# Optimization experiments

Measured on AMD Instinct MI355X. Metric: run time of the kernel, lower is better.

The kernel has to match this reference:

```python
import jax, jax.numpy as jnp
import numpy as np


def _gelu(x):
    # torch nn.GELU default is the exact (erf) variant
    return jax.nn.gelu(x, approximate=False)


def setup_inputs() -> dict:
    key = jax.random.key(0)
    ks = jax.random.split(key, 10)
    B, IN, H, D, C, K = 32768, 64, 256, 16, 8, 64
    HS = D // 2  # structure_filter hidden (latent_dim > 2)

    def rn(k, shape, scale):
        return jax.random.normal(k, shape, dtype=jnp.float32) * scale

    x = rn(ks[0], (B, IN), 1.0)
    W1 = rn(ks[1], (IN, H), 1.0 / np.sqrt(IN)); b1 = jnp.zeros((H,), jnp.float32)
    W2 = rn(ks[2], (H, H), 1.0 / np.sqrt(H));   b2 = jnp.zeros((H,), jnp.float32)
    Wv = rn(ks[3], (H, D), 1.0 / np.sqrt(H));   bv = jnp.zeros((D,), jnp.float32)
    chart_centers = rn(ks[4], (C, D), 0.02)
    codebook = rn(ks[5], (C, K, D), 0.02)
    sf_W1 = rn(ks[6], (D, HS), 1.0 / np.sqrt(D));  sf_b1 = jnp.zeros((HS,), jnp.float32)
    sf_W2 = rn(ks[7], (HS, D), 1.0 / np.sqrt(HS)); sf_b2 = jnp.zeros((D,), jnp.float32)
    return {
        "x": x, "W1": W1, "b1": b1, "W2": W2, "b2": b2, "Wv": Wv, "bv": bv,
        "chart_centers": chart_centers, "codebook": codebook,
        "sf_W1": sf_W1, "sf_b1": sf_b1, "sf_W2": sf_W2, "sf_b2": sf_b2,
    }


def reference(x, W1, b1, W2, b2, Wv, bv, chart_centers, codebook, sf_W1, sf_b1, sf_W2, sf_b2):
    sg = jax.lax.stop_gradient
    # feature extractor: Linear -> GELU -> Linear -> GELU
    f = _gelu(x @ W1 + b1)
    f = _gelu(f @ W2 + b2)
    v = f @ Wv + bv                                        # [B, D]
    D = v.shape[-1]
    C = codebook.shape[0]
    # chart routing
    scores = (v @ chart_centers.T) / jnp.sqrt(jnp.float32(D))   # [B, C]
    router_weights = jax.nn.softmax(scores, axis=-1)
    K_chart = jnp.argmax(router_weights, axis=1)                 # [B]
    c_bar = router_weights @ chart_centers                       # [B, D]
    v_local = v - c_bar
    # per-chart codebook distances
    diff = v_local[:, None, None, :] - codebook[None]            # [B, C, K, D]
    dist = jnp.sum(diff * diff, axis=-1)                         # [B, C, K]
    indices = jnp.argmin(dist, axis=-1)                          # [B, C]
    z_q_all = codebook[jnp.arange(C)[None, :], indices]          # [B, C, D]
    # VQ losses (router weights detached)
    w = sg(router_weights)[:, :, None]                           # [B, C, 1]
    v_bc = v_local[:, None, :]                                   # [B, 1, D]
    commitment = jnp.sum(jnp.mean((v_bc - sg(z_q_all)) ** 2 * w, axis=(0, 2)))
    codebook_loss = jnp.sum(jnp.mean((z_q_all - sg(v_bc)) ** 2 * w, axis=(0, 2)))
    vq_loss = codebook_loss + 0.25 * commitment
    z_q_blended = jnp.sum(z_q_all * router_weights[:, :, None], axis=1)   # [B, D]
    K_code = jnp.take_along_axis(indices, K_chart[:, None], axis=1)[:, 0]  # [B]
    # structure filter on per-chart residuals
    delta = v_bc - sg(z_q_all)                                   # [B, C, D]
    z_n_all_charts = _gelu(delta @ sf_W1 + sf_b1) @ sf_W2 + sf_b2  # [B, C, D]
    z_n = jnp.sum(z_n_all_charts * router_weights[:, :, None], axis=1)
    z_tex = (v_local - sg(z_q_blended)) - z_n
    z_q_st = v_local + sg(z_q_blended - v_local)                 # straight-through
    z_geo = c_bar + z_q_st + z_n
    return (K_chart, K_code, z_n, z_tex, router_weights, z_geo, vq_loss,
            indices, z_n_all_charts, c_bar)
```

## Files before the change

### kernel.cpp

```cpp
#include <hip/hip_runtime.h>
#include <hip/hip_bf16.h>

#define O0 0ull
#define O1 32768ull
#define O2 65536ull
#define O3 589824ull
#define O4 1114112ull
#define O5 1376256ull
#define O6 1900544ull
#define O7 1900545ull
#define O8 2162689ull
#define O9 6356993ull

static constexpr int    ENI  = 16;
static constexpr int    END  = 10;
static constexpr double EW   = 4.27 / 16.0;
static constexpr double EIW  = 16.0 / 4.27;

struct ErfTab { double a[ENI][END]; };

static constexpr double cexp_pos_(double x) {
    double s = 1.0, term = 1.0;
    for (int n = 1; n < 200; ++n) {
        term = term * x / (double)n;
        s += term;
        if (term < 1e-22 * s) break;
    }
    return s;
}
static constexpr ErfTab make_erftab_() {
    ErfTab T{};
    const double k2p = 1.12837916709551257390;
    double c0 = 0.5 * EW;
    double erf_cur = 0.0;
    {
        double u = c0 * c0, term = c0, s = 0.0;
        for (int n = 0; n < 40; ++n) { s += term / (double)(2 * n + 1); term *= -u / (double)(n + 1); }
        erf_cur = k2p * s;
    }
    const int NS = 24;
    for (int i = 0; i < ENI; ++i) {
        double c = ((double)i + 0.5) * EW;
        double e2 = k2p / cexp_pos_(c * c);
        double H[NS]; double a[NS + 1];
        H[0] = 1.0; H[1] = 2.0 * c;
        for (int n = 2; n < NS; ++n) H[n] = 2.0 * c * H[n - 1] - 2.0 * (double)(n - 1) * H[n - 2];
        a[0] = erf_cur;
        double fact = 1.0;
        for (int n = 1; n <= NS; ++n) {
            fact *= (double)n;
            double sgn = ((n - 1) & 1) ? -1.0 : 1.0;
            a[n] = sgn * H[n - 1] * e2 / fact;
        }
        for (int j = 0; j < END; ++j) T.a[i][j] = a[j];
        double s = 0.0, hp = 1.0;
        for (int n = 0; n <= NS; ++n) { s += a[n] * hp; hp *= EW; }
        erf_cur = s;
    }
    return T;
}
__constant__ ErfTab G_ERFTAB = make_erftab_();

__device__ __forceinline__ float erf_np_t(float t, const double* se) {
#pragma clang fp contract(off)
    double x = fabs((double)t);
    int idx = (int)(x * EIW);
    idx = idx > 15 ? 15 : idx;
    const double* A = se + idx * END;
    double d = x - ((double)idx + 0.5) * EW;
    double2 a89 = *(const double2*)(A + 8);
    double2 a67 = *(const double2*)(A + 6);
    double2 a45 = *(const double2*)(A + 4);
    double2 a23 = *(const double2*)(A + 2);
    double2 a01 = *(const double2*)(A + 0);
    double p = a89.y;
    p = fma(p, d, a89.x);
    p = fma(p, d, a67.y); p = fma(p, d, a67.x);
    p = fma(p, d, a45.y); p = fma(p, d, a45.x);
    p = fma(p, d, a23.y); p = fma(p, d, a23.x);
    p = fma(p, d, a01.y); p = fma(p, d, a01.x);
    float e = (x >= 4.1) ? 1.0f : (float)p;
    return (t < 0.0f) ? -e : e;
}

__device__ __forceinline__ float4 gelu4_np(float4 z, const double* se) {
#pragma clang fp contract(off)
    const float s2 = 0x1.6a09e6p+0f;
    float4 r;
    float e0 = erf_np_t(z.x / s2, se);
    float e1 = erf_np_t(z.y / s2, se);
    float e2 = erf_np_t(z.z / s2, se);
    float e3 = erf_np_t(z.w / s2, se);
    r.x = (z.x * (e0 + 1.0f)) / 2.0f;
    r.y = (z.y * (e1 + 1.0f)) / 2.0f;
    r.z = (z.z * (e2 + 1.0f)) / 2.0f;
    r.w = (z.w * (e3 + 1.0f)) / 2.0f;
    return r;
}

__global__ __launch_bounds__(256) void fused_mlp_np_k(
    const float* __restrict__ x,  const float* __restrict__ W1,
    const float* __restrict__ b1, const float* __restrict__ W2,
    const float* __restrict__ b2, const float* __restrict__ Wv,
    const float* __restrict__ bv, float* __restrict__ vout)
{
#pragma clang fp contract(off)
    __shared__ float  ft[16][260];
    __shared__ double serf[ENI * END];
    const int t  = threadIdx.x;
    const int w  = t >> 6;
    const int cg = t & 63;
    const int r0 = blockIdx.x * 16;
    const int rb = w * 4;

    if (t < ENI * END) serf[t] = ((const double*)&G_ERFTAB)[t];
    __syncthreads();

    float acc[4][4];
#pragma unroll
    for (int i = 0; i < 4; ++i) { acc[i][0]=0.f; acc[i][1]=0.f; acc[i][2]=0.f; acc[i][3]=0.f; }

    auto ldw1 = [&](int k) { return *(const float4*)(W1 + (size_t)k * 256 + cg * 4); };
    auto ldw2 = [&](int k) { return *(const float4*)(W2 + (size_t)k * 256 + cg * 4); };

    auto fmaA = [&](int K0, float4 w0, float4 w1_, float4 w2_, float4 w3_) {
#pragma unroll
        for (int rr = 0; rr < 4; ++rr) {
            float4 a = *(const float4*)(x + (size_t)(r0 + rb + rr) * 64 + K0);
            acc[rr][0] = fmaf(a.x, w0.x, acc[rr][0]);
            acc[rr][1] = fmaf(a.x, w0.y, acc[rr][1]);
            acc[rr][2] = fmaf(a.x, w0.z, acc[rr][2]);
            acc[rr][3] = fmaf(a.x, w0.w, acc[rr][3]);
            acc[rr][0] = fmaf(a.y, w1_.x, acc[rr][0]);
            acc[rr][1] = fmaf(a.y, w1_.y, acc[rr][1]);
            acc[rr][2] = fmaf(a.y, w1_.z, acc[rr][2]);
            acc[rr][3] = fmaf(a.y, w1_.w, acc[rr][3]);
            acc[rr][0] = fmaf(a.z, w2_.x, acc[rr][0]);
            acc[rr][1] = fmaf(a.z, w2_.y, acc[rr][1]);
            acc[rr][2] = fmaf(a.z, w2_.z, acc[rr][2]);
            acc[rr][3] = fmaf(a.z, w2_.w, acc[rr][3]);
            acc[rr][0] = fmaf(a.w, w3_.x, acc[rr][0]);
            acc[rr][1] = fmaf(a.w, w3_.y, acc[rr][1]);
            acc[rr][2] = fmaf(a.w, w3_.z, acc[rr][2]);
            acc[rr][3] = fmaf(a.w, w3_.w, acc[rr][3]);
        }
    };
    auto fmaB = [&](int K0, float4 w0, float4 w1_, float4 w2_, float4 w3_) {
#pragma unroll
        for (int rr = 0; rr < 4; ++rr) {
            float4 a = *(const float4*)&ft[rb + rr][K0];
            acc[rr][0] = fmaf(a.x, w0.x, acc[rr][0]);
            acc[rr][1] = fmaf(a.x, w0.y, acc[rr][1]);
            acc[rr][2] = fmaf(a.x, w0.z, acc[rr][2]);
            acc[rr][3] = fmaf(a.x, w0.w, acc[rr][3]);
            acc[rr][0] = fmaf(a.y, w1_.x, acc[rr][0]);
            acc[rr][1] = fmaf(a.y, w1_.y, acc[rr][1]);
            acc[rr][2] = fmaf(a.y, w1_.z, acc[rr][2]);
            acc[rr][3] = fmaf(a.y, w1_.w, acc[rr][3]);
            acc[rr][0] = fmaf(a.z, w2_.x, acc[rr][0]);
            acc[rr][1] = fmaf(a.z, w2_.y, acc[rr][1]);
            acc[rr][2] = fmaf(a.z, w2_.z, acc[rr][2]);
            acc[rr][3] = fmaf(a.z, w2_.w, acc[rr][3]);
            acc[rr][0] = fmaf(a.w, w3_.x, acc[rr][0]);
            acc[rr][1] = fmaf(a.w, w3_.y, acc[rr][1]);
            acc[rr][2] = fmaf(a.w, w3_.z, acc[rr][2]);
            acc[rr][3] = fmaf(a.w, w3_.w, acc[rr][3]);
        }
    };

    {
        float4 u0 = ldw1(0), u1 = ldw1(1), u2 = ldw1(2), u3 = ldw1(3);
        for (int k0 = 0; k0 < 64; k0 += 8) {
            float4 n0 = ldw1(k0 + 4), n1 = ldw1(k0 + 5), n2 = ldw1(k0 + 6), n3 = ldw1(k0 + 7);
            fmaA(k0, u0, u1, u2, u3);
            int kn = (k0 + 8) & 63;
            u0 = ldw1(kn); u1 = ldw1(kn + 1); u2 = ldw1(kn + 2); u3 = ldw1(kn + 3);
            fmaA(k0 + 4, n0, n1, n2, n3);
        }
        float4 bb = *(const float4*)(b1 + cg * 4);
#pragma unroll
        for (int rr = 0; rr < 4; ++rr) {
            float4 z = make_float4(acc[rr][0] + bb.x, acc[rr][1] + bb.y,
                                   acc[rr][2] + bb.z, acc[rr][3] + bb.w);
            *(float4*)&ft[rb + rr][cg * 4] = gelu4_np(z, serf);
        }
    }

#pragma unroll
    for (int i = 0; i < 4; ++i) { acc[i][0]=0.f; acc[i][1]=0.f; acc[i][2]=0.f; acc[i][3]=0.f; }
    {
        float4 u0 = ldw2(0), u1 = ldw2(1), u2 = ldw2(2), u3 = ldw2(3);
        for (int k0 = 0; k0 < 256; k0 += 8) {
            float4 n0 = ldw2(k0 + 4), n1 = ldw2(k0 + 5), n2 = ldw2(k0 + 6), n3 = ldw2(k0 + 7);
            fmaB(k0, u0, u1, u2, u3);
            int kn = (k0 + 8) & 255;
            u0 = ldw2(kn); u1 = ldw2(kn + 1); u2 = ldw2(kn + 2); u3 = ldw2(kn + 3);
            fmaB(k0 + 4, n0, n1, n2, n3);
        }
        float4 bb = *(const float4*)(b2 + cg * 4);
#pragma unroll
        for (int rr = 0; rr < 4; ++rr) {
            float4 z = make_float4(acc[rr][0] + bb.x, acc[rr][1] + bb.y,
                                   acc[rr][2] + bb.z, acc[rr][3] + bb.w);
            *(float4*)&ft[rb + rr][cg * 4] = gelu4_np(z, serf);
        }
    }
    __syncthreads();

    {
        const int vrow = t >> 4;
        const int d    = t & 15;
        float a0 = 0.f;
        for (int k = 0; k < 256; ++k)
            a0 = fmaf(ft[vrow][k], Wv[(size_t)k * 16 + d], a0);
        vout[(size_t)(r0 + vrow) * 16 + d] = a0 + bv[d];
    }
}

__global__ __launch_bounds__(256) void atlas_np_k(
    const float* __restrict__ vbuf, const float* __restrict__ cc,
    const float* __restrict__ cb,   const float* __restrict__ sfW1,
    const float* __restrict__ sfb1, const float* __restrict__ sfW2,
    const float* __restrict__ sfb2, float* __restrict__ out,
    float* __restrict__ partials)
{
#pragma clang fp contract(off)
    __shared__ float scb[8448];
    __shared__ float scc[128];
    __shared__ float sW1[128];
    __shared__ float sW2[128];
    __shared__ float sb1[8];
    __shared__ float sb2[16];
    __shared__ float red[4];
    __shared__ double serf[ENI * END];

    const int t = threadIdx.x;
    for (int i = t; i < 8192; i += 256) {
        int c = i >> 10, rem = i & 1023, kk = rem >> 4, d = rem & 15;
        scb[c * 1032 + kk * 16 + d] = cb[i];
    }
    if (t < 128) { scc[t] = cc[t]; sW1[t] = sfW1[t]; sW2[t] = sfW2[t]; }
    if (t < 8)  sb1[t] = sfb1[t];
    if (t < 16) sb2[t] = sfb2[t];
    if (t >= 64 && t < 64 + ENI * END) serf[t - 64] = ((const double*)&G_ERFTAB)[t - 64];
    __syncthreads();

    const int c    = t & 7;
    const int rloc = t >> 3;
    const int lane = t & 63;
    const int lb   = lane & ~7;
    const int row  = blockIdx.x * 32 + rloc;

    float v[16];
    {
        const float4* vp = (const float4*)(vbuf + (size_t)row * 16);
        float4 a = vp[0], b = vp[1], g = vp[2], h4 = vp[3];
        v[0]=a.x;  v[1]=a.y;  v[2]=a.z;  v[3]=a.w;
        v[4]=b.x;  v[5]=b.y;  v[6]=b.z;  v[7]=b.w;
        v[8]=g.x;  v[9]=g.y;  v[10]=g.z; v[11]=g.w;
        v[12]=h4.x; v[13]=h4.y; v[14]=h4.z; v[15]=h4.w;
    }

    float score = 0.f;
#pragma unroll
    for (int d = 0; d < 16; ++d) score = fmaf(v[d], scc[c * 16 + d], score);
    score = score / 4.0f;

    float m = score;
#pragma unroll
    for (int off = 1; off < 8; off <<= 1) m = fmaxf(m, __shfl_xor(m, off));
    float e = (float)exp((double)(score - m));
    float ea[8];
#pragma unroll
    for (int j = 0; j < 8; ++j) ea[j] = __shfl(e, lb + j);
    float s = ((ea[0] + ea[1]) + (ea[2] + ea[3])) + ((ea[4] + ea[5]) + (ea[6] + ea[7]));
    float rw = e / s;

    float rwa[8];
#pragma unroll
    for (int j = 0; j < 8; ++j) rwa[j] = ea[j] / s;

    float bmv = rwa[0]; int bci = 0;
#pragma unroll
    for (int j = 1; j < 8; ++j) if (rwa[j] > bmv) { bmv = rwa[j]; bci = j; }

    float cbar[16], vl[16];
#pragma unroll
    for (int d = 0; d < 16; ++d) {
        float a = 0.f;
#pragma unroll
        for (int j = 0; j < 8; ++j) a = fmaf(rwa[j], scc[j * 16 + d], a);
        cbar[d] = a;
        vl[d]   = v[d] - a;
    }

    const float* cbc = scb + c * 1032;
    float bd = 3.4e38f; int bk = 0; bool first = true;
    for (int kk = 0; kk < 64; ++kk) {
        const float4* q = (const float4*)(cbc + kk * 16);
        float4 q0 = q[0], q1 = q[1], q2 = q[2], q3 = q[3];
        float sq[16];
        float dd;
        dd = vl[0]  - q0.x; sq[0]  = dd * dd;
        dd = vl[1]  - q0.y; sq[1]  = dd * dd;
        dd = vl[2]  - q0.z; sq[2]  = dd * dd;
        dd = vl[3]  - q0.w; sq[3]  = dd * dd;
        dd = vl[4]  - q1.x; sq[4]  = dd * dd;
        dd = vl[5]  - q1.y; sq[5]  = dd * dd;
        dd = vl[6]  - q1.z; sq[6]  = dd * dd;
        dd = vl[7]  - q1.w; sq[7]  = dd * dd;
        dd = vl[8]  - q2.x; sq[8]  = dd * dd;
        dd = vl[9]  - q2.y; sq[9]  = dd * dd;
        dd = vl[10] - q2.z; sq[10] = dd * dd;
        dd = vl[11] - q2.w; sq[11] = dd * dd;
        dd = vl[12] - q3.x; sq[12] = dd * dd;
        dd = vl[13] - q3.y; sq[13] = dd * dd;
        dd = vl[14] - q3.z; sq[14] = dd * dd;
        dd = vl[15] - q3.w; sq[15] = dd * dd;
        float r0_ = sq[0] + sq[8],  r1_ = sq[1] + sq[9];
        float r2_ = sq[2] + sq[10], r3_ = sq[3] + sq[11];
        float r4_ = sq[4] + sq[12], r5_ = sq[5] + sq[13];
        float r6_ = sq[6] + sq[14], r7_ = sq[7] + sq[15];
        float dist = ((r0_ + r1_) + (r2_ + r3_)) + ((r4_ + r5_) + (r6_ + r7_));
        if (first || dist < bd) { bd = dist; bk = kk; first = false; }
    }

    float zq[16];
    {
        const float4* q = (const float4*)(cbc + bk * 16);
        float4 q0 = q[0], q1 = q[1], q2 = q[2], q3 = q[3];
        zq[0]=q0.x;  zq[1]=q0.y;  zq[2]=q0.z;  zq[3]=q0.w;
        zq[4]=q1.x;  zq[5]=q1.y;  zq[6]=q1.z;  zq[7]=q1.w;
        zq[8]=q2.x;  zq[9]=q2.y;  zq[10]=q2.z; zq[11]=q2.w;
        zq[12]=q3.x; zq[13]=q3.y; zq[14]=q3.z; zq[15]=q3.w;
    }

    float del[16];
#pragma unroll
    for (int d = 0; d < 16; ++d) del[d] = vl[d] - zq[d];

    float pa[8];
#pragma unroll
    for (int j = 0; j < 8; ++j) {
        float a = 0.f;
#pragma unroll
        for (int d = 0; d < 16; ++d) a = fmaf(del[d], sW1[d * 8 + j], a);
        pa[j] = a + sb1[j];
    }
    float4 g0 = gelu4_np(make_float4(pa[0], pa[1], pa[2], pa[3]), serf);
    float4 g1 = gelu4_np(make_float4(pa[4], pa[5], pa[6], pa[7]), serf);
    float h[8] = { g0.x, g0.y, g0.z, g0.w, g1.x, g1.y, g1.z, g1.w };

    float zn[16];
#pragma unroll
    for (int d = 0; d < 16; ++d) {
        float a = 0.f;
#pragma unroll
        for (int j = 0; j < 8; ++j) a = fmaf(h[j], sW2[j * 16 + d], a);
        zn[d] = a + sb2[d];
    }

    float ls = 0.f;
#pragma unroll
    for (int d = 0; d < 16; ++d) ls = fmaf(del[d], del[d], ls);
    ls *= rw;

    __syncthreads();
    float* zql = scb;
    float* znl = scb + 4224;
    {
        float* pq = zql + rloc * 132 + c * 16;
        float* pn = znl + rloc * 132 + c * 16;
        *(float4*)&pq[0]  = make_float4(zq[0],  zq[1],  zq[2],  zq[3]);
        *(float4*)&pq[4]  = make_float4(zq[4],  zq[5],  zq[6],  zq[7]);
        *(float4*)&pq[8]  = make_float4(zq[8],  zq[9],  zq[10], zq[11]);
        *(float4*)&pq[12] = make_float4(zq[12], zq[13], zq[14], zq[15]);
        *(float4*)&pn[0]  = make_float4(zn[0],  zn[1],  zn[2],  zn[3]);
        *(float4*)&pn[4]  = make_float4(zn[4],  zn[5],  zn[6],  zn[7]);
        *(float4*)&pn[8]  = make_float4(zn[8],  zn[9],  zn[10], zn[11]);
        *(float4*)&pn[12] = make_float4(zn[12], zn[13], zn[14], zn[15]);
    }
    __syncthreads();

    const int dd0 = c * 2;
    float aq0 = 0.f, aq1 = 0.f, an0 = 0.f, an1 = 0.f;
#pragma unroll
    for (int j = 0; j < 8; ++j) {
        float2 qv = *(const float2*)&zql[rloc * 132 + j * 16 + dd0];
        float2 nv = *(const float2*)&znl[rloc * 132 + j * 16 + dd0];
        float p0 = qv.x * rwa[j]; aq0 = aq0 + p0;
        float p1 = qv.y * rwa[j]; aq1 = aq1 + p1;
        float p2 = nv.x * rwa[j]; an0 = an0 + p2;
        float p3 = nv.y * rwa[j]; an1 = an1 + p3;
    }

    out[O4 + (size_t)row * 8 + c] = rw;
    out[O7 + (size_t)row * 8 + c] = (float)bk;
    {
        float* p = out + O8 + (size_t)row * 128 + c * 16;
#pragma unroll
        for (int d = 0; d < 16; ++d) p[d] = zn[d];
    }
    if (c == 0)   out[O0 + row] = (float)bci;
    if (c == bci) out[O1 + row] = (float)bk;
    {
        int d = dd0;
        float zst0 = vl[d]     + (aq0 - vl[d]);
        float zst1 = vl[d + 1] + (aq1 - vl[d + 1]);
        out[O2 + (size_t)row * 16 + d]     = an0;
        out[O2 + (size_t)row * 16 + d + 1] = an1;
        out[O3 + (size_t)row * 16 + d]     = (vl[d]     - aq0) - an0;
        out[O3 + (size_t)row * 16 + d + 1] = (vl[d + 1] - aq1) - an1;
        out[O5 + (size_t)row * 16 + d]     = (cbar[d]     + zst0) + an0;
        out[O5 + (size_t)row * 16 + d + 1] = (cbar[d + 1] + zst1) + an1;
        out[O9 + (size_t)row * 16 + d]     = cbar[d];
        out[O9 + (size_t)row * 16 + d + 1] = cbar[d + 1];
    }

#pragma unroll
    for (int off = 1; off < 64; off <<= 1) ls += __shfl_xor(ls, off);
    if ((t & 63) == 0) red[t >> 6] = ls;
    __syncthreads();
    if (t == 0) partials[blockIdx.x] = red[0] + red[1] + red[2] + red[3];
}

__global__ __launch_bounds__(256) void loss_reduce_k(
    const float* __restrict__ partials, float* __restrict__ out)
{
    __shared__ float sm[256];
    const int t = threadIdx.x;
    float a = 0.f;
    for (int i = t; i < 1024; i += 256) a += partials[i];
    sm[t] = a;
    __syncthreads();
    for (int s2 = 128; s2 > 0; s2 >>= 1) {
        if (t < s2) sm[t] += sm[t + s2];
        __syncthreads();
    }
    if (t == 0) out[O6] = sm[0] * (1.25f / 524288.0f);
}

extern "C" void kernel_launch(void* const* d_in, const int* in_sizes, int n_in,
                              void* d_out, int out_size, void* d_ws, size_t ws_size,
                              hipStream_t stream) {
    (void)in_sizes; (void)n_in; (void)out_size;
    const float* x    = (const float*)d_in[0];
    const float* W1   = (const float*)d_in[1];
    const float* b1   = (const float*)d_in[2];
    const float* W2   = (const float*)d_in[3];
    const float* b2   = (const float*)d_in[4];
    const float* Wv   = (const float*)d_in[5];
    const float* bv   = (const float*)d_in[6];
    const float* cc   = (const float*)d_in[7];
    const float* cb   = (const float*)d_in[8];
    const float* sfW1 = (const float*)d_in[9];
    const float* sfb1 = (const float*)d_in[10];
    const float* sfW2 = (const float*)d_in[11];
    const float* sfb2 = (const float*)d_in[12];
    float* out = (float*)d_out;

    float* vbuf = (float*)d_ws;
    float* partials = vbuf + (size_t)32768 * 16;
    if (ws_size < ((size_t)32768 * 16 + 1024) * 4) return;

    fused_mlp_np_k<<<2048, 256, 0, stream>>>(x, W1, b1, W2, b2, Wv, bv, vbuf);
    atlas_np_k    <<<1024, 256, 0, stream>>>(vbuf, cc, cb, sfW1, sfb1, sfW2, sfb2, out, partials);
    loss_reduce_k <<<1, 256, 0, stream>>>(partials, out);
}
```

Baseline: 167.7 us.

## Stage W1/W2 weight chunks through double-buffered shared memory

Weight rows of W1 and W2 used to be loaded directly from global memory by every wave, so the four waves of a block each fetched the same data. Now the block cooperatively loads 16-row chunks of W1 and then W2 into a two-slot shared-memory buffer. The next chunk is prefetched into registers while the current one is being computed. This removes redundant global and cache traffic for the weights, at the cost of a block barrier per chunk and about 32 KB of extra LDS per block, which may lower occupancy.

```diff
diff --git a/kernel.cpp b/kernel.cpp
--- a/kernel.cpp
+++ b/kernel.cpp
@@ -106,6 +106,7 @@
 {
 #pragma clang fp contract(off)
     __shared__ float  ft[16][260];
+    __shared__ float  wbuf[2][4096];
     __shared__ double serf[ENI * END];
     const int t  = threadIdx.x;
     const int w  = t >> 6;
@@ -114,69 +115,92 @@
     const int rb = w * 4;
 
     if (t < ENI * END) serf[t] = ((const double*)&G_ERFTAB)[t];
-    __syncthreads();
 
     float acc[4][4];
 #pragma unroll
     for (int i = 0; i < 4; ++i) { acc[i][0]=0.f; acc[i][1]=0.f; acc[i][2]=0.f; acc[i][3]=0.f; }
 
-    auto ldw1 = [&](int k) { return *(const float4*)(W1 + (size_t)k * 256 + cg * 4); };
-    auto ldw2 = [&](int k) { return *(const float4*)(W2 + (size_t)k * 256 + cg * 4); };
-
-    auto fmaA = [&](int K0, float4 w0, float4 w1_, float4 w2_, float4 w3_) {
-#pragma unroll
-        for (int rr = 0; rr < 4; ++rr) {
-            float4 a = *(const float4*)(x + (size_t)(r0 + rb + rr) * 64 + K0);
-            acc[rr][0] = fmaf(a.x, w0.x, acc[rr][0]);
-            acc[rr][1] = fmaf(a.x, w0.y, acc[rr][1]);
-            acc[rr][2] = fmaf(a.x, w0.z, acc[rr][2]);
-            acc[rr][3] = fmaf(a.x, w0.w, acc[rr][3]);
-            acc[rr][0] = fmaf(a.y, w1_.x, acc[rr][0]);
-            acc[rr][1] = fmaf(a.y, w1_.y, acc[rr][1]);
-            acc[rr][2] = fmaf(a.y, w1_.z, acc[rr][2]);
-            acc[rr][3] = fmaf(a.y, w1_.w, acc[rr][3]);
-            acc[rr][0] = fmaf(a.z, w2_.x, acc[rr][0]);
-            acc[rr][1] = fmaf(a.z, w2_.y, acc[rr][1]);
-            acc[rr][2] = fmaf(a.z, w2_.z, acc[rr][2]);
-            acc[rr][3] = fmaf(a.z, w2_.w, acc[rr][3]);
-            acc[rr][0] = fmaf(a.w, w3_.x, acc[rr][0]);
-            acc[rr][1] = fmaf(a.w, w3_.y, acc[rr][1]);
-            acc[rr][2] = fmaf(a.w, w3_.z, acc[rr][2]);
-            acc[rr][3] = fmaf(a.w, w3_.w, acc[rr][3]);
+    float4 st[4];
+
+    auto ld_chunk = [&](const float* M, int c) {
+        const float4* src = (const float4*)(M + (size_t)c * 4096);
+#pragma unroll
+        for (int j = 0; j < 4; ++j) st[j] = src[t + j * 256];
+    };
+    auto wr_chunk = [&](int b) {
+        float4* dst = (float4*)wbuf[b];
+#pragma unroll
+        for (int j = 0; j < 4; ++j) dst[t + j * 256] = st[j];
+    };
+
+    auto computeA = [&](int c, int b) {
+#pragma unroll
+        for (int kk = 0; kk < 16; kk += 4) {
+            float4 w0 = *(const float4*)&wbuf[b][(kk + 0) * 256 + cg * 4];
+            float4 w1_ = *(const float4*)&wbuf[b][(kk + 1) * 256 + cg * 4];
+            float4 w2_ = *(const float4*)&wbuf[b][(kk + 2) * 256 + cg * 4];
+            float4 w3_ = *(const float4*)&wbuf[b][(kk + 3) * 256 + cg * 4];
+#pragma unroll
+            for (int rr = 0; rr < 4; ++rr) {
+                float4 a = *(const float4*)(x + (size_t)(r0 + rb + rr) * 64 + c * 16 + kk);
+                acc[rr][0] = fmaf(a.x, w0.x, acc[rr][0]);
+                acc[rr][1] = fmaf(a.x, w0.y, acc[rr][1]);
+                acc[rr][2] = fmaf(a.x, w0.z, acc[rr][2]);
+                acc[rr][3] = fmaf(a.x, w0.w, acc[rr][3]);
+                acc[rr][0] = fmaf(a.y, w1_.x, acc[rr][0]);
+                acc[rr][1] = fmaf(a.y, w1_.y, acc[rr][1]);
+                acc[rr][2] = fmaf(a.y, w1_.z, acc[rr][2]);
+                acc[rr][3] = fmaf(a.y, w1_.w, acc[rr][3]);
+                acc[rr][0] = fmaf(a.z, w2_.x, acc[rr][0]);
+                acc[rr][1] = fmaf(a.z, w2_.y, acc[rr][1]);
+                acc[rr][2] = fmaf(a.z, w2_.z, acc[rr][2]);
+                acc[rr][3] = fmaf(a.z, w2_.w, acc[rr][3]);
+                acc[rr][0] = fmaf(a.w, w3_.x, acc[rr][0]);
+                acc[rr][1] = fmaf(a.w, w3_.y, acc[rr][1]);
+                acc[rr][2] = fmaf(a.w, w3_.z, acc[rr][2]);
+                acc[rr][3] = fmaf(a.w, w3_.w, acc[rr][3]);
+            }
         }
     };
-    auto fmaB = [&](int K0, float4 w0, float4 w1_, float4 w2_, float4 w3_) {
-#pragma unroll
-        for (int rr = 0; rr < 4; ++rr) {
-            float4 a = *(const float4*)&ft[rb + rr][K0];
-            acc[rr][0] = fmaf(a.x, w0.x, acc[rr][0]);
-            acc[rr][1] = fmaf(a.x, w0.y, acc[rr][1]);
-            acc[rr][2] = fmaf(a.x, w0.z, acc[rr][2]);
-            acc[rr][3] = fmaf(a.x, w0.w, acc[rr][3]);
-            acc[rr][0] = fmaf(a.y, w1_.x, acc[rr][0]);
-            acc[rr][1] = fmaf(a.y, w1_.y, acc[rr][1]);
-            acc[rr][2] = fmaf(a.y, w1_.z, acc[rr][2]);
-            acc[rr][3] = fmaf(a.y, w1_.w, acc[rr][3]);
-            acc[rr][0] = fmaf(a.z, w2_.x, acc[rr][0]);
-            acc[rr][1] = fmaf(a.z, w2_.y, acc[rr][1]);
-            acc[rr][2] = fmaf(a.z, w2_.z, acc[rr][2]);
-            acc[rr][3] = fmaf(a.z, w2_.w, acc[rr][3]);
-            acc[rr][0] = fmaf(a.w, w3_.x, acc[rr][0]);
-            acc[rr][1] = fmaf(a.w, w3_.y, acc[rr][1]);
-            acc[rr][2] = fmaf(a.w, w3_.z, acc[rr][2]);
-            acc[rr][3] = fmaf(a.w, w3_.w, acc[rr][3]);
+    auto computeB = [&](int c, int b) {
+#pragma unroll
+        for (int kk = 0; kk < 16; kk += 4) {
+            float4 w0 = *(const float4*)&wbuf[b][(kk + 0) * 256 + cg * 4];
+            float4 w1_ = *(const float4*)&wbuf[b][(kk + 1) * 256 + cg * 4];
+            float4 w2_ = *(const float4*)&wbuf[b][(kk + 2) * 256 + cg * 4];
+            float4 w3_ = *(const float4*)&wbuf[b][(kk + 3) * 256 + cg * 4];
+#pragma unroll
+            for (int rr = 0; rr < 4; ++rr) {
+                float4 a = *(const float4*)&ft[rb + rr][c * 16 + kk];
+                acc[rr][0] = fmaf(a.x, w0.x, acc[rr][0]);
+                acc[rr][1] = fmaf(a.x, w0.y, acc[rr][1]);
+                acc[rr][2] = fmaf(a.x, w0.z, acc[rr][2]);
+                acc[rr][3] = fmaf(a.x, w0.w, acc[rr][3]);
+                acc[rr][0] = fmaf(a.y, w1_.x, acc[rr][0]);
+                acc[rr][1] = fmaf(a.y, w1_.y, acc[rr][1]);
+                acc[rr][2] = fmaf(a.y, w1_.z, acc[rr][2]);
+                acc[rr][3] = fmaf(a.y, w1_.w, acc[rr][3]);
+                acc[rr][0] = fmaf(a.z, w2_.x, acc[rr][0]);
+                acc[rr][1] = fmaf(a.z, w2_.y, acc[rr][1]);
+                acc[rr][2] = fmaf(a.z, w2_.z, acc[rr][2]);
+                acc[rr][3] = fmaf(a.z, w2_.w, acc[rr][3]);
+                acc[rr][0] = fmaf(a.w, w3_.x, acc[rr][0]);
+                acc[rr][1] = fmaf(a.w, w3_.y, acc[rr][1]);
+                acc[rr][2] = fmaf(a.w, w3_.z, acc[rr][2]);
+                acc[rr][3] = fmaf(a.w, w3_.w, acc[rr][3]);
+            }
         }
     };
 
-    {
-        float4 u0 = ldw1(0), u1 = ldw1(1), u2 = ldw1(2), u3 = ldw1(3);
-        for (int k0 = 0; k0 < 64; k0 += 8) {
-            float4 n0 = ldw1(k0 + 4), n1 = ldw1(k0 + 5), n2 = ldw1(k0 + 6), n3 = ldw1(k0 + 7);
-            fmaA(k0, u0, u1, u2, u3);
-            int kn = (k0 + 8) & 63;
-            u0 = ldw1(kn); u1 = ldw1(kn + 1); u2 = ldw1(kn + 2); u3 = ldw1(kn + 3);
-            fmaA(k0 + 4, n0, n1, n2, n3);
-        }
+    ld_chunk(W1, 0);
+    for (int c = 0; c < 4; ++c) {
+        wr_chunk(c & 1);
+        __syncthreads();
+        if (c < 3) ld_chunk(W1, c + 1);
+        else       ld_chunk(W2, 0);
+        computeA(c, c & 1);
+    }
+    {
         float4 bb = *(const float4*)(b1 + cg * 4);
 #pragma unroll
         for (int rr = 0; rr < 4; ++rr) {
@@ -188,15 +212,13 @@
 
 #pragma unroll
     for (int i = 0; i < 4; ++i) { acc[i][0]=0.f; acc[i][1]=0.f; acc[i][2]=0.f; acc[i][3]=0.f; }
-    {
-        float4 u0 = ldw2(0), u1 = ldw2(1), u2 = ldw2(2), u3 = ldw2(3);
-        for (int k0 = 0; k0 < 256; k0 += 8) {
-            float4 n0 = ldw2(k0 + 4), n1 = ldw2(k0 + 5), n2 = ldw2(k0 + 6), n3 = ldw2(k0 + 7);
-            fmaB(k0, u0, u1, u2, u3);
-            int kn = (k0 + 8) & 255;
-            u0 = ldw2(kn); u1 = ldw2(kn + 1); u2 = ldw2(kn + 2); u3 = ldw2(kn + 3);
-            fmaB(k0 + 4, n0, n1, n2, n3);
-        }
+    for (int c = 0; c < 16; ++c) {
+        wr_chunk(c & 1);
+        __syncthreads();
+        if (c < 15) ld_chunk(W2, c + 1);
+        computeB(c, c & 1);
+    }
+    {
         float4 bb = *(const float4*)(b2 + cg * 4);
 #pragma unroll
         for (int rr = 0; rr < 4; ++rr) {
```

After: 262.0 us. 56.2% more time.
